# Kernel optimization log

Measured on AMD Instinct MI355X. Metric: run time of the kernel, lower is better.

Reference implementation:

```python
import jax, jax.numpy as jnp
import numpy as np

DIM = 1024
N_HEADS = 16
HEAD_DIM = DIM // N_HEADS
LORA_DIM = 16
B, T = 4, 1024


def _rope(x):
    # x: [B, H, T, D] with D even; rotate first/second halves (torch impl style)
    D = x.shape[-1]
    half = D // 2
    theta = 1.0 / (10000.0 ** (jnp.arange(0, D, 2, dtype=jnp.float32) / D))  # [D/2]
    pos = jnp.arange(x.shape[-2], dtype=jnp.float32)                         # [T]
    pt = pos[:, None] * theta[None, :]                                       # [T, D/2]
    sin, cos = jnp.sin(pt), jnp.cos(pt)
    xr, xi = x[..., :half], x[..., half:]
    return jnp.concatenate([xr * cos - xi * sin, xr * sin + xi * cos], axis=-1)


def setup_inputs() -> dict:
    key = jax.random.key(0)
    ks = jax.random.split(key, 16)
    def n(k, shape, std=0.02):
        return jax.random.normal(k, shape, jnp.float32) * std
    return {
        "x": jax.random.normal(ks[0], (B, T, DIM), jnp.float32),
        "q_w": n(ks[1], (DIM, DIM)),
        "k_w": n(ks[2], (DIM, DIM)),
        "v_w": n(ks[3], (DIM, DIM)),
        "q_a": n(ks[4], (LORA_DIM, DIM), 0.001),
        "q_b": n(ks[5], (DIM, LORA_DIM), 0.001),
        "q_l": jax.random.normal(ks[6], (DIM,), jnp.float32),
        "k_a": n(ks[7], (LORA_DIM, DIM), 0.001),
        "k_b": n(ks[8], (DIM, LORA_DIM), 0.001),
        "k_l": jax.random.normal(ks[9], (DIM,), jnp.float32),
        "v_a": n(ks[10], (LORA_DIM, DIM), 0.001),
        "v_b": n(ks[11], (DIM, LORA_DIM), 0.001),
        "v_l": jax.random.normal(ks[12], (DIM,), jnp.float32),
        "proj_w": n(ks[13], (DIM, DIM)),
        "proj_b": n(ks[14], (DIM,)),
    }


def reference(x, q_w, k_w, v_w, q_a, q_b, q_l, k_a, k_b, k_l,
              v_a, v_b, v_l, proj_w, proj_b):
    Bb, Tt, C = x.shape
    # token shift: xx[t] = x[t-1], xx[0] = 0 (ZeroPad2d((0,0,1,-1)))
    xx = jnp.pad(x, ((0, 0), (1, 0), (0, 0)))[:, :Tt]
    xxx = xx - x

    def lora(a, b, lam):
        return lam + jnp.tanh(x @ a.T) @ b.T  # [B,T,C]

    q = (x + xxx * lora(q_a, q_b, q_l)) @ q_w.T
    k = (x + xxx * lora(k_a, k_b, k_l)) @ k_w.T
    v = (x + xxx * lora(v_a, v_b, v_l)) @ v_w.T

    def split_heads(t):
        return t.reshape(Bb, Tt, N_HEADS, HEAD_DIM).transpose(0, 2, 1, 3)  # [B,H,T,D]

    q = _rope(split_heads(q))
    k = _rope(split_heads(k))
    v = split_heads(v)

    scale = 1.0 / np.sqrt(HEAD_DIM).astype(np.float32)
    scores = jnp.einsum('bhqd,bhkd->bhqk', q, k) * scale
    causal = jnp.tril(jnp.ones((Tt, Tt), dtype=bool))
    scores = jnp.where(causal, scores, jnp.float32(-1e30))
    att = jax.nn.softmax(scores, axis=-1)
    out = jnp.einsum('bhqk,bhkd->bhqd', att, v)
    out = out.transpose(0, 2, 1, 3).reshape(Bb, Tt, C)
    return out @ proj_w.T + proj_b
```

## Files before the change

kernel.cpp:

```cpp
#include <hip/hip_runtime.h>
#include <hip/hip_bf16.h>

typedef __hip_bfloat16 bf16;
typedef __attribute__((ext_vector_type(8))) short bf16x8;
typedef __attribute__((ext_vector_type(4))) float f32x4;

typedef const __attribute__((address_space(1))) unsigned int* gp_t;
typedef __attribute__((address_space(3))) unsigned int* lp_t;

__device__ __forceinline__ bf16 tobf(float f) { return __float2bfloat16(f); }
__device__ __forceinline__ float tof(bf16 h) { return __bfloat162float(h); }

__device__ __forceinline__ short bfbits(float f) {
    bf16 h = __float2bfloat16(f);
    return *reinterpret_cast<short*>(&h);
}
__device__ __forceinline__ bf16x8 pack8(float4 a, float4 b) {
    bf16x8 r;
    r[0] = bfbits(a.x); r[1] = bfbits(a.y); r[2] = bfbits(a.z); r[3] = bfbits(a.w);
    r[4] = bfbits(b.x); r[5] = bfbits(b.y); r[6] = bfbits(b.z); r[7] = bfbits(b.w);
    return r;
}

__device__ __forceinline__ void gload_lds16(const void* g, void* l) {
    __builtin_amdgcn_global_load_lds((gp_t)g, (lp_t)l, 16, 0, 0);
}

__global__ __launch_bounds__(256) void convert_w(const float* qw, const float* kw,
                                                 const float* vw, const float* pw,
                                                 bf16* dst) {
    int m = blockIdx.y;
    const float* src = m == 0 ? qw : (m == 1 ? kw : (m == 2 ? vw : pw));
    bf16* d = dst + (size_t)m * (1u << 20);
    int i = (blockIdx.x * 256 + threadIdx.x) * 4;
    float4 f = *(const float4*)(src + i);
    d[i + 0] = tobf(f.x);
    d[i + 1] = tobf(f.y);
    d[i + 2] = tobf(f.z);
    d[i + 3] = tobf(f.w);
}

__global__ __launch_bounds__(256) void lora_gate_fused(
    const float* x,
    const float* qa, const float* ka, const float* va,
    const float* qbw, const float* ql,
    const float* kbw, const float* kl,
    const float* vbw, const float* vl,
    bf16* xqo, bf16* xko, bf16* xvo) {
    const int XS = 1028;
    int row0 = blockIdx.x * 16;
    int t0 = row0 & 1023;
    int tid = threadIdx.x;
    int wave = tid >> 6, lane = tid & 63;
    int quad = lane >> 4, l16 = lane & 15;

    __shared__ float sx[17 * 1028];
    __shared__ float sT[16 * 48];

    {
        int prow = (row0 == 0) ? 0 : row0 - 1;
        for (int i = 0; i < 17; ++i) {
            int grow = (i == 0) ? prow : row0 + i - 1;
            gload_lds16(x + (size_t)grow * 1024 + wave * 256 + lane * 4,
                        &sx[i * XS + wave * 256]);
        }
    }
    __syncthreads();

    if (wave < 3) {
        const float* am = wave == 0 ? qa : (wave == 1 ? ka : va);
        f32x4 acc = (f32x4){0.f, 0.f, 0.f, 0.f};
#pragma unroll 4
        for (int k0 = 0; k0 < 1024; k0 += 32) {
            const float* xs = &sx[(1 + l16) * XS + k0 + quad * 8];
            bf16x8 af = pack8(*(const float4*)xs, *(const float4*)(xs + 4));
            const float* as = am + (size_t)l16 * 1024 + k0 + quad * 8;
            bf16x8 bf_ = pack8(*(const float4*)as, *(const float4*)(as + 4));
            acc = __builtin_amdgcn_mfma_f32_16x16x32_bf16(af, bf_, acc, 0, 0, 0);
        }
#pragma unroll
        for (int r = 0; r < 4; ++r)
            sT[(quad * 4 + r) * 48 + wave * 16 + l16] = tanhf(acc[r]);
    }
    __syncthreads();

#pragma unroll
    for (int u = 0; u < 4; ++u) {
        int d = tid + u * 256;
        float qbv[16], kbv[16], vbv[16];
#pragma unroll
        for (int p = 0; p < 4; ++p) {
            *(float4*)&qbv[p * 4] = *(const float4*)(qbw + (size_t)d * 16 + p * 4);
            *(float4*)&kbv[p * 4] = *(const float4*)(kbw + (size_t)d * 16 + p * 4);
            *(float4*)&vbv[p * 4] = *(const float4*)(vbw + (size_t)d * 16 + p * 4);
        }
        float qlv = ql[d], klv = kl[d], vlv = vl[d];
        float xp = (t0 == 0) ? 0.f : sx[0 * XS + d];
        for (int rr = 0; rr < 16; ++rr) {
            float xc = sx[(rr + 1) * XS + d];
            float dx = xp - xc;
            float gq = qlv, gk = klv, gv = vlv;
#pragma unroll
            for (int j = 0; j < 16; ++j) {
                gq += sT[rr * 48 + j] * qbv[j];
                gk += sT[rr * 48 + 16 + j] * kbv[j];
                gv += sT[rr * 48 + 32 + j] * vbv[j];
            }
            size_t o = (size_t)(row0 + rr) * 1024 + d;
            xqo[o] = tobf(xc + dx * gq);
            xko[o] = tobf(xc + dx * gk);
            xvo[o] = tobf(xc + dx * gv);
            xp = xc;
        }
    }
}

__global__ __launch_bounds__(256) void gemm128(
    const bf16* A0, const bf16* A1, const bf16* A2,
    const bf16* W0, const bf16* W1, const bf16* W2,
    bf16* C0, bf16* C1, bf16* C2,
    const float* bias, float* outF, int proj, int zcnt) {
    const int K = 1024;
    int ppx = (zcnt * 32) >> 3;
    int xcd = blockIdx.x & 7;
    int j = blockIdx.x >> 3;
    int pair = xcd * ppx + (j >> 3);
    int n0 = (j & 7) * 128;
    int bz = pair >> 5;
    int m0 = (pair & 31) * 128;

    const bf16* A = bz == 0 ? A0 : (bz == 1 ? A1 : A2);
    const bf16* W = bz == 0 ? W0 : (bz == 1 ? W1 : W2);
    bf16* C = bz == 0 ? C0 : (bz == 1 ? C1 : C2);

    __shared__ alignas(16) bf16 sA[128 * 64];
    __shared__ alignas(16) bf16 sB[128 * 64];

    int wave = threadIdx.x >> 6, lane = threadIdx.x & 63;
    int quad = lane >> 4, l16 = lane & 15;
    int m7 = l16 & 7;

    f32x4 acc[4][4];
#pragma unroll
    for (int i = 0; i < 4; i++)
#pragma unroll
        for (int j2 = 0; j2 < 4; j2++) acc[i][j2] = (f32x4){0.f, 0.f, 0.f, 0.f};

    int srow = lane >> 3;
    int scol = ((lane & 7) ^ srow) * 8;

    int mw = (wave >> 1) * 64, nw = (wave & 1) * 64;

    for (int k0 = 0; k0 < K; k0 += 64) {
        __syncthreads();
#pragma unroll
        for (int p = 0; p < 4; p++) {
            int rbase = wave * 32 + p * 8;
            gload_lds16(A + (size_t)(m0 + rbase + srow) * K + k0 + scol, &sA[rbase * 64]);
            gload_lds16(W + (size_t)(n0 + rbase + srow) * K + k0 + scol, &sB[rbase * 64]);
        }
        __syncthreads();
#pragma unroll
        for (int ks = 0; ks < 2; ks++) {
            bf16x8 af[4], bfr[4];
#pragma unroll
            for (int f = 0; f < 4; f++) {
                int c = ((quad + ks * 4) ^ m7) * 8;
                af[f] = *(const bf16x8*)&sA[(mw + f * 16 + l16) * 64 + c];
                bfr[f] = *(const bf16x8*)&sB[(nw + f * 16 + l16) * 64 + c];
            }
#pragma unroll
            for (int i = 0; i < 4; i++)
#pragma unroll
                for (int j2 = 0; j2 < 4; j2++)
                    acc[i][j2] = __builtin_amdgcn_mfma_f32_16x16x32_bf16(af[i], bfr[j2], acc[i][j2], 0, 0, 0);
        }
    }

#pragma unroll
    for (int i = 0; i < 4; i++) {
        int mrow = m0 + mw + i * 16 + quad * 4;
#pragma unroll
        for (int j2 = 0; j2 < 4; j2++) {
            int col = n0 + nw + j2 * 16 + l16;
            if (proj) {
                float bv = bias[col];
#pragma unroll
                for (int r = 0; r < 4; r++)
                    outF[(size_t)(mrow + r) * 1024 + col] = acc[i][j2][r] + bv;
            } else {
#pragma unroll
                for (int r = 0; r < 4; r++)
                    C[(size_t)(mrow + r) * 1024 + col] = tobf(acc[i][j2][r]);
            }
        }
    }
}

__global__ __launch_bounds__(256) void rope_transform(
    const bf16* q, const bf16* k, const bf16* v,
    bf16* Qh, bf16* Kh, bf16* Vt) {
    int bh = blockIdx.x, tblk = blockIdx.y;
    int b = bh >> 4, h = bh & 15;
    int t0 = tblk * 64;
    int tid = threadIdx.x;

    int i0 = (tid & 7) * 4;
#pragma unroll
    for (int pp = 0; pp < 2; ++pp) {
        int t = t0 + pp * 32 + (tid >> 3);
        size_t gin = ((size_t)(b * 1024 + t)) * 1024 + h * 64;
        size_t gout = ((size_t)(bh * 1024 + t)) * 64;
        float c[4], s[4];
#pragma unroll
        for (int u = 0; u < 4; ++u) {
            int i = i0 + u;
            float theta = __expf(-(float)i * (9.210340371976184f / 32.0f));
            sincosf((float)t * theta, &s[u], &c[u]);
        }
        float xr[4], xi[4];
#pragma unroll
        for (int u = 0; u < 4; u++) { xr[u] = tof(q[gin + i0 + u]); xi[u] = tof(q[gin + 32 + i0 + u]); }
#pragma unroll
        for (int u = 0; u < 4; u++) {
            Qh[gout + i0 + u]      = tobf((xr[u] * c[u] - xi[u] * s[u]) * 0.125f);
            Qh[gout + 32 + i0 + u] = tobf((xr[u] * s[u] + xi[u] * c[u]) * 0.125f);
        }
#pragma unroll
        for (int u = 0; u < 4; u++) { xr[u] = tof(k[gin + i0 + u]); xi[u] = tof(k[gin + 32 + i0 + u]); }
#pragma unroll
        for (int u = 0; u < 4; u++) {
            Kh[gout + i0 + u]      = tobf(xr[u] * c[u] - xi[u] * s[u]);
            Kh[gout + 32 + i0 + u] = tobf(xr[u] * s[u] + xi[u] * c[u]);
        }
    }

    __shared__ bf16 sv[64 * 65];
    {
        int r = tid >> 2;
        int c0 = (tid & 3) * 16;
        size_t g = ((size_t)(b * 1024 + t0 + r)) * 1024 + h * 64 + c0;
#pragma unroll
        for (int u = 0; u < 16; u++) sv[(c0 + u) * 65 + r] = v[g + u];
    }
    __syncthreads();
    {
        int d = tid >> 2;
        int tc = (tid & 3) * 16;
        size_t g = ((size_t)(bh * 64 + d)) * 1024 + t0 + tc;
#pragma unroll
        for (int u = 0; u < 16; u++) Vt[g + u] = sv[d * 65 + tc + u];
    }
}

__global__ __launch_bounds__(256) void attention(const bf16* Qh, const bf16* Kh,
                                                 const bf16* Vt, bf16* attn) {
    int gid = blockIdx.x;
    int qblk = 15 - (gid >> 6);
    int bh = (((gid >> 3) & 7) << 3) | (gid & 7);
    int b = bh >> 4, h = bh & 15;
    int wave = threadIdx.x >> 6, lane = threadIdx.x & 63;
    int quad = lane >> 4, l16 = lane & 15;
    int m7 = l16 & 7;

    const bf16* Qb = Qh + (size_t)bh * 1024 * 64;
    const bf16* Kb = Kh + (size_t)bh * 1024 * 64;
    const bf16* Vb = Vt + (size_t)bh * 64 * 1024;

    __shared__ alignas(16) bf16 sK[2][64 * 64];
    __shared__ alignas(16) bf16 sV[2][64 * 64];
    __shared__ alignas(16) bf16 sP[4][16 * 64];

    int srow = lane >> 3;
    int scol = ((lane & 7) ^ srow) * 8;

    auto stage = [&](int kt, int bufi) {
#pragma unroll
        for (int p = 0; p < 2; p++) {
            int rbase = p * 32 + wave * 8;
            gload_lds16(Kb + (size_t)(kt * 64 + rbase + srow) * 64 + scol, &sK[bufi][rbase * 64]);
            gload_lds16(Vb + (size_t)(rbase + srow) * 1024 + kt * 64 + scol, &sV[bufi][rbase * 64]);
        }
    };

    int qrow0 = qblk * 64 + wave * 16;
    bf16x8 aq0 = *(const bf16x8*)&Qb[(size_t)(qrow0 + l16) * 64 + quad * 8];
    bf16x8 aq1 = *(const bf16x8*)&Qb[(size_t)(qrow0 + l16) * 64 + quad * 8 + 32];

    f32x4 o[4];
#pragma unroll
    for (int nt = 0; nt < 4; nt++) o[nt] = (f32x4){0.f, 0.f, 0.f, 0.f};
    float mrow[4], lrow[4];
#pragma unroll
    for (int r = 0; r < 4; r++) { mrow[r] = -3.0e38f; lrow[r] = 0.f; }

    stage(0, 0);

    int buf = 0;
    for (int kt = 0; kt <= qblk; ++kt, buf ^= 1) {
        __syncthreads();
        if (kt < qblk) stage(kt + 1, buf ^ 1);

        f32x4 S[4];
#pragma unroll
        for (int j = 0; j < 4; j++) {
            int row = j * 16 + l16;
            bf16x8 bk0 = *(const bf16x8*)&sK[buf][row * 64 + ((quad ^ m7) * 8)];
            bf16x8 bk1 = *(const bf16x8*)&sK[buf][row * 64 + (((quad + 4) ^ m7) * 8)];
            f32x4 z = __builtin_amdgcn_mfma_f32_16x16x32_bf16(aq0, bk0, (f32x4){0.f, 0.f, 0.f, 0.f}, 0, 0, 0);
            S[j] = __builtin_amdgcn_mfma_f32_16x16x32_bf16(aq1, bk1, z, 0, 0, 0);
        }
        if (kt == qblk) {
#pragma unroll
            for (int j = 0; j < 4; j++) {
                int key = kt * 64 + j * 16 + l16;
#pragma unroll
                for (int r = 0; r < 4; r++) {
                    int qr = qrow0 + quad * 4 + r;
                    if (key > qr) S[j][r] = -3.0e38f;
                }
            }
        }
        float alpha[4];
#pragma unroll
        for (int r = 0; r < 4; r++) {
            float vmax = fmaxf(fmaxf(S[0][r], S[1][r]), fmaxf(S[2][r], S[3][r]));
            vmax = fmaxf(vmax, __shfl_xor(vmax, 1));
            vmax = fmaxf(vmax, __shfl_xor(vmax, 2));
            vmax = fmaxf(vmax, __shfl_xor(vmax, 4));
            vmax = fmaxf(vmax, __shfl_xor(vmax, 8));
            float mn = fmaxf(mrow[r], vmax);
            alpha[r] = __expf(mrow[r] - mn);
            mrow[r] = mn;
        }
        float rs[4] = {0.f, 0.f, 0.f, 0.f};
#pragma unroll
        for (int j = 0; j < 4; j++)
#pragma unroll
            for (int r = 0; r < 4; r++) {
                float p = __expf(S[j][r] - mrow[r]);
                S[j][r] = p;
                rs[r] += p;
            }
#pragma unroll
        for (int r = 0; r < 4; r++) {
            float v = rs[r];
            v += __shfl_xor(v, 1);
            v += __shfl_xor(v, 2);
            v += __shfl_xor(v, 4);
            v += __shfl_xor(v, 8);
            lrow[r] = lrow[r] * alpha[r] + v;
        }
#pragma unroll
        for (int nt = 0; nt < 4; nt++)
#pragma unroll
            for (int r = 0; r < 4; r++) o[nt][r] *= alpha[r];

#pragma unroll
        for (int j = 0; j < 4; j++) {
            int c = j * 2 + (l16 >> 3);
#pragma unroll
            for (int r = 0; r < 4; r++) {
                int prow = quad * 4 + r;
                sP[wave][prow * 64 + ((c ^ (prow & 7)) * 8) + m7] = tobf(S[j][r]);
            }
        }
        asm volatile("s_waitcnt lgkmcnt(0)" ::: "memory");
        bf16x8 ap0 = *(const bf16x8*)&sP[wave][l16 * 64 + ((quad ^ m7) * 8)];
        bf16x8 ap1 = *(const bf16x8*)&sP[wave][l16 * 64 + (((quad + 4) ^ m7) * 8)];
#pragma unroll
        for (int nt = 0; nt < 4; nt++) {
            int row = nt * 16 + l16;
            bf16x8 bv0 = *(const bf16x8*)&sV[buf][row * 64 + ((quad ^ m7) * 8)];
            bf16x8 bv1 = *(const bf16x8*)&sV[buf][row * 64 + (((quad + 4) ^ m7) * 8)];
            o[nt] = __builtin_amdgcn_mfma_f32_16x16x32_bf16(ap0, bv0, o[nt], 0, 0, 0);
            o[nt] = __builtin_amdgcn_mfma_f32_16x16x32_bf16(ap1, bv1, o[nt], 0, 0, 0);
        }
    }

    float invl[4];
#pragma unroll
    for (int r = 0; r < 4; r++) invl[r] = 1.0f / lrow[r];
#pragma unroll
    for (int nt = 0; nt < 4; nt++)
#pragma unroll
        for (int r = 0; r < 4; r++) {
            int t = qrow0 + quad * 4 + r;
            int col = h * 64 + nt * 16 + l16;
            attn[(size_t)(b * 1024 + t) * 1024 + col] = tobf(o[nt][r] * invl[r]);
        }
}

extern "C" void kernel_launch(void* const* d_in, const int* in_sizes, int n_in,
                              void* d_out, int out_size, void* d_ws, size_t ws_size,
                              hipStream_t stream) {
    const float* x = (const float*)d_in[0];
    const float* qw = (const float*)d_in[1];
    const float* kw = (const float*)d_in[2];
    const float* vw = (const float*)d_in[3];
    const float* qa = (const float*)d_in[4];
    const float* qb = (const float*)d_in[5];
    const float* ql = (const float*)d_in[6];
    const float* ka = (const float*)d_in[7];
    const float* kb = (const float*)d_in[8];
    const float* kl = (const float*)d_in[9];
    const float* va = (const float*)d_in[10];
    const float* vb = (const float*)d_in[11];
    const float* vl = (const float*)d_in[12];
    const float* pw = (const float*)d_in[13];
    const float* pb = (const float*)d_in[14];
    float* out = (float*)d_out;

    char* ws = (char*)d_ws;
    const size_t MB = 1024 * 1024;
    bf16* wqb = (bf16*)ws;
    bf16* wkb = wqb + 1048576;
    bf16* wvb = wkb + 1048576;
    bf16* wpb = wvb + 1048576;
    bf16* xqb = (bf16*)(ws + 8 * MB);
    bf16* xkb = xqb + 4194304;
    bf16* xvb = xkb + 4194304;
    bf16* qm = (bf16*)(ws + 32 * MB);
    bf16* km = qm + 4194304;
    bf16* vm = km + 4194304;
    bf16* Qh = xqb;
    bf16* Kh = xkb;
    bf16* Vt = xvb;
    bf16* attn = qm;

    convert_w<<<dim3(1024, 4), 256, 0, stream>>>(qw, kw, vw, pw, wqb);
    lora_gate_fused<<<256, 256, 0, stream>>>(x, qa, ka, va, qb, ql, kb, kl, vb, vl,
                                             xqb, xkb, xvb);
    gemm128<<<768, 256, 0, stream>>>(xqb, xkb, xvb, wqb, wkb, wvb, qm, km, vm,
                                     nullptr, nullptr, 0, 3);
    rope_transform<<<dim3(64, 16), 256, 0, stream>>>(qm, km, vm, Qh, Kh, Vt);
    attention<<<1024, 256, 0, stream>>>(Qh, Kh, Vt, attn);
    gemm128<<<256, 256, 0, stream>>>(attn, nullptr, nullptr, wpb, nullptr, nullptr,
                                     nullptr, nullptr, nullptr, pb, out, 1, 1);
}
```

Measured before the change: 234.8 us.

## Fuse RoPE into QKV GEMM epilogue and double-buffer GEMM K loop

The QKV GEMM epilogue now applies RoPE and the 1/8 query scale directly to the accumulators for Q and K. This removes the separate rope pass over Q and K, leaving a kernel that only transposes V. Attention now reads Q and K from the row-major [B,T,C] layout with a stride of 1024. The GEMM main loop changes to a double-buffered 32-wide K stage with a new swizzled LDS layout and a single barrier per iteration. This trades sincos work in the GEMM epilogue and strided Q/K loads in attention for less memory traffic and one fewer round trip.

```diff
diff --git a/kernel.cpp b/kernel.cpp
--- a/kernel.cpp
+++ b/kernel.cpp
@@ -133,12 +133,11 @@
     const bf16* W = bz == 0 ? W0 : (bz == 1 ? W1 : W2);
     bf16* C = bz == 0 ? C0 : (bz == 1 ? C1 : C2);
 
-    __shared__ alignas(16) bf16 sA[128 * 64];
-    __shared__ alignas(16) bf16 sB[128 * 64];
+    __shared__ alignas(16) bf16 sA[2][64 * 64];
+    __shared__ alignas(16) bf16 sB[2][64 * 64];
 
     int wave = threadIdx.x >> 6, lane = threadIdx.x & 63;
     int quad = lane >> 4, l16 = lane & 15;
-    int m7 = l16 & 7;
 
     f32x4 acc[4][4];
 #pragma unroll
@@ -146,49 +145,86 @@
 #pragma unroll
         for (int j2 = 0; j2 < 4; j2++) acc[i][j2] = (f32x4){0.f, 0.f, 0.f, 0.f};
 
-    int srow = lane >> 3;
-    int scol = ((lane & 7) ^ srow) * 8;
+    int Rb0 = wave * 16 + (lane >> 3);
+    int s0 = lane & 7;
+
+    auto stage = [&](int k0, int bufi) {
+#pragma unroll
+        for (int p = 0; p < 2; p++) {
+            int R = Rb0 + p * 8;
+            int cs = s0 ^ (R & 7);
+            int mr = 2 * R + (cs >> 2);
+            int kc = (cs & 3) * 8;
+            gload_lds16(A + (size_t)(m0 + mr) * K + k0 + kc, &sA[bufi][(wave * 16 + p * 8) * 64]);
+            gload_lds16(W + (size_t)(n0 + mr) * K + k0 + kc, &sB[bufi][(wave * 16 + p * 8) * 64]);
+        }
+    };
 
     int mw = (wave >> 1) * 64, nw = (wave & 1) * 64;
-
-    for (int k0 = 0; k0 < K; k0 += 64) {
+    int slot = (((l16 & 1) << 2) | quad) ^ ((l16 >> 1) & 7);
+    int abase = ((mw >> 1) + (l16 >> 1)) * 64 + slot * 8;
+    int bbase = ((nw >> 1) + (l16 >> 1)) * 64 + slot * 8;
+
+    stage(0, 0);
+    for (int it = 0; it < 32; ++it) {
         __syncthreads();
-#pragma unroll
-        for (int p = 0; p < 4; p++) {
-            int rbase = wave * 32 + p * 8;
-            gload_lds16(A + (size_t)(m0 + rbase + srow) * K + k0 + scol, &sA[rbase * 64]);
-            gload_lds16(W + (size_t)(n0 + rbase + srow) * K + k0 + scol, &sB[rbase * 64]);
-        }
-        __syncthreads();
-#pragma unroll
-        for (int ks = 0; ks < 2; ks++) {
-            bf16x8 af[4], bfr[4];
-#pragma unroll
-            for (int f = 0; f < 4; f++) {
-                int c = ((quad + ks * 4) ^ m7) * 8;
-                af[f] = *(const bf16x8*)&sA[(mw + f * 16 + l16) * 64 + c];
-                bfr[f] = *(const bf16x8*)&sB[(nw + f * 16 + l16) * 64 + c];
-            }
-#pragma unroll
-            for (int i = 0; i < 4; i++)
-#pragma unroll
-                for (int j2 = 0; j2 < 4; j2++)
-                    acc[i][j2] = __builtin_amdgcn_mfma_f32_16x16x32_bf16(af[i], bfr[j2], acc[i][j2], 0, 0, 0);
-        }
-    }
-
-#pragma unroll
-    for (int i = 0; i < 4; i++) {
-        int mrow = m0 + mw + i * 16 + quad * 4;
-#pragma unroll
-        for (int j2 = 0; j2 < 4; j2++) {
-            int col = n0 + nw + j2 * 16 + l16;
-            if (proj) {
+        if (it + 1 < 32) stage((it + 1) * 32, (it + 1) & 1);
+        const bf16* pa = sA[it & 1];
+        const bf16* pb = sB[it & 1];
+        bf16x8 af[4], bfr[4];
+#pragma unroll
+        for (int f = 0; f < 4; f++) {
+            af[f] = *(const bf16x8*)&pa[abase + f * 512];
+            bfr[f] = *(const bf16x8*)&pb[bbase + f * 512];
+        }
+#pragma unroll
+        for (int i = 0; i < 4; i++)
+#pragma unroll
+            for (int j2 = 0; j2 < 4; j2++)
+                acc[i][j2] = __builtin_amdgcn_mfma_f32_16x16x32_bf16(af[i], bfr[j2], acc[i][j2], 0, 0, 0);
+    }
+
+    if (proj) {
+#pragma unroll
+        for (int i = 0; i < 4; i++) {
+            int mrow = m0 + mw + i * 16 + quad * 4;
+#pragma unroll
+            for (int j2 = 0; j2 < 4; j2++) {
+                int col = n0 + nw + j2 * 16 + l16;
                 float bv = bias[col];
 #pragma unroll
                 for (int r = 0; r < 4; r++)
                     outF[(size_t)(mrow + r) * 1024 + col] = acc[i][j2][r] + bv;
-            } else {
+            }
+        }
+    } else if (bz < 2) {
+        float sc = (bz == 0) ? 0.125f : 1.0f;
+#pragma unroll
+        for (int i = 0; i < 4; i++) {
+            int mrow = m0 + mw + i * 16 + quad * 4;
+#pragma unroll
+            for (int j2 = 0; j2 < 2; j2++) {
+                int d = j2 * 16 + l16;
+                float theta = __expf(-(float)d * (9.210340371976184f / 32.0f));
+                int col = n0 + nw + j2 * 16 + l16;
+#pragma unroll
+                for (int r = 0; r < 4; r++) {
+                    int t = (mrow + r) & 1023;
+                    float s, c;
+                    sincosf((float)t * theta, &s, &c);
+                    float xr = acc[i][j2][r], xi = acc[i][j2 + 2][r];
+                    C[(size_t)(mrow + r) * 1024 + col] = tobf((xr * c - xi * s) * sc);
+                    C[(size_t)(mrow + r) * 1024 + col + 32] = tobf((xr * s + xi * c) * sc);
+                }
+            }
+        }
+    } else {
+#pragma unroll
+        for (int i = 0; i < 4; i++) {
+            int mrow = m0 + mw + i * 16 + quad * 4;
+#pragma unroll
+            for (int j2 = 0; j2 < 4; j2++) {
+                int col = n0 + nw + j2 * 16 + l16;
 #pragma unroll
                 for (int r = 0; r < 4; r++)
                     C[(size_t)(mrow + r) * 1024 + col] = tobf(acc[i][j2][r]);
@@ -197,43 +233,11 @@
     }
 }
 
-__global__ __launch_bounds__(256) void rope_transform(
-    const bf16* q, const bf16* k, const bf16* v,
-    bf16* Qh, bf16* Kh, bf16* Vt) {
+__global__ __launch_bounds__(256) void v_transpose(const bf16* v, bf16* Vt) {
     int bh = blockIdx.x, tblk = blockIdx.y;
     int b = bh >> 4, h = bh & 15;
     int t0 = tblk * 64;
     int tid = threadIdx.x;
-
-    int i0 = (tid & 7) * 4;
-#pragma unroll
-    for (int pp = 0; pp < 2; ++pp) {
-        int t = t0 + pp * 32 + (tid >> 3);
-        size_t gin = ((size_t)(b * 1024 + t)) * 1024 + h * 64;
-        size_t gout = ((size_t)(bh * 1024 + t)) * 64;
-        float c[4], s[4];
-#pragma unroll
-        for (int u = 0; u < 4; ++u) {
-            int i = i0 + u;
-            float theta = __expf(-(float)i * (9.210340371976184f / 32.0f));
-            sincosf((float)t * theta, &s[u], &c[u]);
-        }
-        float xr[4], xi[4];
-#pragma unroll
-        for (int u = 0; u < 4; u++) { xr[u] = tof(q[gin + i0 + u]); xi[u] = tof(q[gin + 32 + i0 + u]); }
-#pragma unroll
-        for (int u = 0; u < 4; u++) {
-            Qh[gout + i0 + u]      = tobf((xr[u] * c[u] - xi[u] * s[u]) * 0.125f);
-            Qh[gout + 32 + i0 + u] = tobf((xr[u] * s[u] + xi[u] * c[u]) * 0.125f);
-        }
-#pragma unroll
-        for (int u = 0; u < 4; u++) { xr[u] = tof(k[gin + i0 + u]); xi[u] = tof(k[gin + 32 + i0 + u]); }
-#pragma unroll
-        for (int u = 0; u < 4; u++) {
-            Kh[gout + i0 + u]      = tobf(xr[u] * c[u] - xi[u] * s[u]);
-            Kh[gout + 32 + i0 + u] = tobf(xr[u] * s[u] + xi[u] * c[u]);
-        }
-    }
 
     __shared__ bf16 sv[64 * 65];
     {
@@ -253,7 +257,7 @@
     }
 }
 
-__global__ __launch_bounds__(256) void attention(const bf16* Qh, const bf16* Kh,
+__global__ __launch_bounds__(256) void attention(const bf16* Qm, const bf16* Km,
                                                  const bf16* Vt, bf16* attn) {
     int gid = blockIdx.x;
     int qblk = 15 - (gid >> 6);
@@ -263,8 +267,8 @@
     int quad = lane >> 4, l16 = lane & 15;
     int m7 = l16 & 7;
 
-    const bf16* Qb = Qh + (size_t)bh * 1024 * 64;
-    const bf16* Kb = Kh + (size_t)bh * 1024 * 64;
+    const bf16* Qb = Qm + (size_t)b * 1024 * 1024 + h * 64;
+    const bf16* Kb = Km + (size_t)b * 1024 * 1024 + h * 64;
     const bf16* Vb = Vt + (size_t)bh * 64 * 1024;
 
     __shared__ alignas(16) bf16 sK[2][64 * 64];
@@ -278,14 +282,14 @@
 #pragma unroll
         for (int p = 0; p < 2; p++) {
             int rbase = p * 32 + wave * 8;
-            gload_lds16(Kb + (size_t)(kt * 64 + rbase + srow) * 64 + scol, &sK[bufi][rbase * 64]);
+            gload_lds16(Kb + (size_t)(kt * 64 + rbase + srow) * 1024 + scol, &sK[bufi][rbase * 64]);
             gload_lds16(Vb + (size_t)(rbase + srow) * 1024 + kt * 64 + scol, &sV[bufi][rbase * 64]);
         }
     };
 
     int qrow0 = qblk * 64 + wave * 16;
-    bf16x8 aq0 = *(const bf16x8*)&Qb[(size_t)(qrow0 + l16) * 64 + quad * 8];
-    bf16x8 aq1 = *(const bf16x8*)&Qb[(size_t)(qrow0 + l16) * 64 + quad * 8 + 32];
+    bf16x8 aq0 = *(const bf16x8*)&Qb[(size_t)(qrow0 + l16) * 1024 + quad * 8];
+    bf16x8 aq1 = *(const bf16x8*)&Qb[(size_t)(qrow0 + l16) * 1024 + quad * 8 + 32];
 
     f32x4 o[4];
 #pragma unroll
@@ -423,18 +427,16 @@
     bf16* qm = (bf16*)(ws + 32 * MB);
     bf16* km = qm + 4194304;
     bf16* vm = km + 4194304;
-    bf16* Qh = xqb;
-    bf16* Kh = xkb;
     bf16* Vt = xvb;
-    bf16* attn = qm;
+    bf16* attn = xqb;
 
     convert_w<<<dim3(1024, 4), 256, 0, stream>>>(qw, kw, vw, pw, wqb);
     lora_gate_fused<<<256, 256, 0, stream>>>(x, qa, ka, va, qb, ql, kb, kl, vb, vl,
                                              xqb, xkb, xvb);
     gemm128<<<768, 256, 0, stream>>>(xqb, xkb, xvb, wqb, wkb, wvb, qm, km, vm,
                                      nullptr, nullptr, 0, 3);
-    rope_transform<<<dim3(64, 16), 256, 0, stream>>>(qm, km, vm, Qh, Kh, Vt);
-    attention<<<1024, 256, 0, stream>>>(Qh, Kh, Vt, attn);
+    v_transpose<<<dim3(64, 16), 256, 0, stream>>>(vm, Vt);
+    attention<<<1024, 256, 0, stream>>>(qm, km, Vt, attn);
     gemm128<<<256, 256, 0, stream>>>(attn, nullptr, nullptr, wpb, nullptr, nullptr,
                                      nullptr, nullptr, nullptr, pb, out, 1, 1);
 }
```

Result: no change. 238.4 us (+1.5%).
